# Kernel optimization log

Measured on AMD Instinct MI355X. Metric: run time of the kernel, lower is better.

Reference implementation:

```python
import jax, jax.numpy as jnp
import numpy as np

HIDDEN = 1024
SCALE = float(np.sqrt(HIDDEN))  # canonical sqrt(d) scale factor


def setup_inputs() -> dict:
    key = jax.random.key(0)
    ks = jax.random.split(key, 10)
    B, S, D = 4, 2048, HIDDEN
    bound = 1.0 / np.sqrt(D)  # torch Linear default init range
    inp = {
        "q": jax.random.normal(ks[0], (B, S, D), dtype=jnp.float32),
        "k": jax.random.normal(ks[1], (B, S, D), dtype=jnp.float32),
        "v": jax.random.normal(ks[2], (B, S, D), dtype=jnp.float32),
        "mask": jnp.zeros((B, S, S), dtype=bool),  # unused by original forward
        "Wq": jax.random.uniform(ks[3], (D, D), jnp.float32, -bound, bound),
        "bq": jax.random.uniform(ks[4], (D,), jnp.float32, -bound, bound),
        "Wk": jax.random.uniform(ks[5], (D, D), jnp.float32, -bound, bound),
        "bk": jax.random.uniform(ks[6], (D,), jnp.float32, -bound, bound),
        "Wv": jax.random.uniform(ks[7], (D, D), jnp.float32, -bound, bound),
        "bv": jax.random.uniform(ks[8], (D,), jnp.float32, -bound, bound),
    }
    return inp


def reference(q, k, v, mask, Wq, bq, Wk, bk, Wv, bv):
    # torch Linear: y = x @ W.T + b
    qp = jnp.einsum("bsd,ed->bse", q, Wq) + bq  # [B,S,D]
    kp = jnp.einsum("bsd,ed->bse", k, Wk) + bk
    vp = jnp.einsum("bsd,ed->bse", v, Wv) + bv
    scores = jnp.einsum("bqd,bkd->bqk", qp, kp) / SCALE  # [B,S,S]
    attn = jax.nn.softmax(scores, axis=-1)
    # dropout with p=0 (dropout_p undefined in source) -> identity
    out = jnp.einsum("bqk,bkd->bqd", attn, vp)  # [B,S,D]
    return out
```

## Files before the change

### kernel.cpp

```cpp
#include <hip/hip_runtime.h>

#define S_ 2048
#define D_ 1024
#define MTOT 8192

typedef __attribute__((ext_vector_type(8))) short bf16x8;
typedef __attribute__((ext_vector_type(8))) unsigned short ush8;
typedef __attribute__((ext_vector_type(4))) unsigned short ush4;
typedef __attribute__((ext_vector_type(4))) float f32x4;

__device__ __forceinline__ unsigned short f2bf(float x) {
    unsigned u = __builtin_bit_cast(unsigned, x);
    u += 0x7fffu + ((u >> 16) & 1u);
    return (unsigned short)(u >> 16);
}

__device__ __forceinline__ void async16(const unsigned short* g, unsigned short* l) {
    __builtin_amdgcn_global_load_lds(
        (const __attribute__((address_space(1))) unsigned int*)(g),
        (__attribute__((address_space(3))) unsigned int*)(l),
        16, 0, 0);
}

#define FENCE() asm volatile("" ::: "memory")
#define SBAR()  __builtin_amdgcn_s_barrier()
#define SCHED0() __builtin_amdgcn_sched_barrier(0)

template<int N> __device__ __forceinline__ void waitv();
template<> __device__ __forceinline__ void waitv<0>() { asm volatile("s_waitcnt vmcnt(0)" ::: "memory"); }
template<> __device__ __forceinline__ void waitv<6>() { asm volatile("s_waitcnt vmcnt(6)" ::: "memory"); }
template<> __device__ __forceinline__ void waitv<8>() { asm volatile("s_waitcnt vmcnt(8)" ::: "memory"); }

__device__ __forceinline__ int xcd_remap(int id, int nwg) {
    return (id & 7) * (nwg >> 3) + (id >> 3);
}

__global__ __launch_bounds__(256)
void tobf16_kernel(const float* __restrict__ s0, const float* __restrict__ s1,
                   const float* __restrict__ s2, const float* __restrict__ s3,
                   const float* __restrict__ s4, const float* __restrict__ s5,
                   const float* __restrict__ bq, const float* __restrict__ bk,
                   const float* __restrict__ bv,
                   unsigned short* __restrict__ d0, unsigned short* __restrict__ d1,
                   unsigned short* __restrict__ d2, unsigned short* __restrict__ d3,
                   unsigned short* __restrict__ d4, unsigned short* __restrict__ d5,
                   float* __restrict__ bias_out)
{
    if (blockIdx.y == 6) {
        if (blockIdx.x != 0) return;
        const int t = threadIdx.x;
        for (int i = t; i < 768; i += 256) {
            const int fidx = i * 4;
            const float* src = (fidx < 1024) ? bq : (fidx < 2048) ? bk : bv;
            reinterpret_cast<float4*>(bias_out)[i] =
                reinterpret_cast<const float4*>(src)[(fidx & 1023) >> 2];
        }
        return;
    }
    const float* src; unsigned short* dst; size_t n;
    switch (blockIdx.y) {
        case 0: src = s0; dst = d0; n = (size_t)MTOT * D_; break;
        case 1: src = s1; dst = d1; n = (size_t)MTOT * D_; break;
        case 2: src = s2; dst = d2; n = (size_t)MTOT * D_; break;
        case 3: src = s3; dst = d3; n = (size_t)D_ * D_;   break;
        case 4: src = s4; dst = d4; n = (size_t)D_ * D_;   break;
        default: src = s5; dst = d5; n = (size_t)D_ * D_;  break;
    }
    size_t base = ((size_t)blockIdx.x * 256 + threadIdx.x) * 8;
    if (base >= n) return;
    float4 a = *reinterpret_cast<const float4*>(src + base);
    float4 b = *reinterpret_cast<const float4*>(src + base + 4);
    ush8 h;
    h[0] = f2bf(a.x); h[1] = f2bf(a.y); h[2] = f2bf(a.z); h[3] = f2bf(a.w);
    h[4] = f2bf(b.x); h[5] = f2bf(b.y); h[6] = f2bf(b.z); h[7] = f2bf(b.w);
    *reinterpret_cast<ush8*>(dst + base) = h;
}

template<int EPI, int BM>
__device__ __forceinline__ void gemm_body(
    unsigned short* As, unsigned short* Bs,
    const unsigned short* __restrict__ Ag, int lda,
    const unsigned short* __restrict__ Bg, int ldb,
    const float* __restrict__ bias,
    float* __restrict__ Cf, unsigned short* __restrict__ Cbf,
    int K, float alpha, int ldc, int m0, int n0, size_t coff)
{
    constexpr int WM    = BM / 2;
    constexpr int MI    = WM / 16;
    constexpr int RQ    = MI / 4;
    constexpr int ASLAB = BM / 64;
    constexpr int SC    = ASLAB + 4;
    constexpr int ABUF  = BM * 64;
    constexpr int BBUF  = 256 * 64;

    const int t = threadIdx.x;
    const int w = t >> 6, lane = t & 63;
    const int wr = w >> 2, wc = w & 3;
    const int lr = lane & 15, lk4 = lane >> 4;

    const int crow = t >> 3;
    const int cj = ((lane & 7) ^ ((lane >> 4) & 3) ^ (((lane >> 3) & 1) << 2)) * 8;

    auto stA = [&](int buf, int s, int kt) {
        async16(Ag + (size_t)(m0 + s * 64 + crow) * lda + kt * 64 + cj,
                As + buf * ABUF + s * 4096 + w * 512);
    };
    auto stB = [&](int buf, int s, int kt) {
        async16(Bg + (size_t)(n0 + s * 64 + crow) * ldb + kt * 64 + cj,
                Bs + buf * BBUF + s * 4096 + w * 512);
    };
    auto rdA = [&](int buf, int rr, int kk) -> bf16x8 {
        const int phys = ((kk * 4 + lk4) ^ ((rr >> 1) & 3) ^ ((rr & 1) << 2)) * 8;
        return *reinterpret_cast<const bf16x8*>(As + buf * ABUF + rr * 64 + phys);
    };
    auto rdB = [&](int buf, int rr, int kk) -> bf16x8 {
        const int phys = ((kk * 4 + lk4) ^ ((rr >> 1) & 3) ^ ((rr & 1) << 2)) * 8;
        return *reinterpret_cast<const bf16x8*>(Bs + buf * BBUF + rr * 64 + phys);
    };

    f32x4 acc[MI][4];
    const f32x4 z4 = {0.f, 0.f, 0.f, 0.f};
#pragma unroll
    for (int i = 0; i < MI; i++)
#pragma unroll
        for (int j = 0; j < 4; j++) acc[i][j] = z4;

    const int NT = K >> 6;

#pragma unroll
    for (int s = 0; s < ASLAB; ++s) stA(0, s, 0);
#pragma unroll
    for (int s = 0; s < 4; ++s)     stB(0, s, 0);
#pragma unroll
    for (int s = 0; s < ASLAB; ++s) stA(1, s, 1);
#pragma unroll
    for (int s = 0; s < 4; ++s)     stB(1, s, 1);
    waitv<SC>(); SCHED0(); SBAR(); FENCE();

    for (int kt = 0; kt < NT; ++kt) {
        const int cur = kt & 1;
        const bool pf = (kt + 2 < NT);

        bf16x8 bfr[4][2];
        bf16x8 af[RQ][2];

#pragma unroll
        for (int ni = 0; ni < 4; ++ni)
#pragma unroll
            for (int kk = 0; kk < 2; ++kk)
                bfr[ni][kk] = rdB(cur, wc * 64 + ni * 16 + lr, kk);
#pragma unroll
        for (int rr = 0; rr < RQ; ++rr)
#pragma unroll
            for (int kk = 0; kk < 2; ++kk)
                af[rr][kk] = rdA(cur, wr * WM + rr * 16 + lr, kk);
        FENCE(); SBAR();
        __builtin_amdgcn_s_setprio(1);
#pragma unroll
        for (int rr = 0; rr < RQ; ++rr)
#pragma unroll
            for (int ni = 0; ni < 4; ++ni)
#pragma unroll
                for (int kk = 0; kk < 2; ++kk)
                    acc[rr][ni] = __builtin_amdgcn_mfma_f32_16x16x32_bf16(af[rr][kk], bfr[ni][kk], acc[rr][ni], 0, 0, 0);
        __builtin_amdgcn_s_setprio(0);
        FENCE(); SBAR();

#pragma unroll
        for (int q = 1; q < 4; ++q) {
#pragma unroll
            for (int rr = 0; rr < RQ; ++rr)
#pragma unroll
                for (int kk = 0; kk < 2; ++kk)
                    af[rr][kk] = rdA(cur, wr * WM + (q * RQ + rr) * 16 + lr, kk);
            if (pf) {
                if (q == 1)      { stB(cur, 0, kt + 2); stB(cur, 1, kt + 2); }
                else if (q == 2) { stB(cur, 2, kt + 2); stB(cur, 3, kt + 2); }
                else if (BM == 256) { stA(cur, 0, kt + 2); stA(cur, 2, kt + 2); }
            }
            FENCE(); SBAR();
            __builtin_amdgcn_s_setprio(1);
#pragma unroll
            for (int rr = 0; rr < RQ; ++rr)
#pragma unroll
                for (int ni = 0; ni < 4; ++ni)
#pragma unroll
                    for (int kk = 0; kk < 2; ++kk)
                        acc[q * RQ + rr][ni] = __builtin_amdgcn_mfma_f32_16x16x32_bf16(af[rr][kk], bfr[ni][kk], acc[q * RQ + rr][ni], 0, 0, 0);
            __builtin_amdgcn_s_setprio(0);
            FENCE(); SBAR();
        }

        if (pf) {
            if (BM == 256) { stA(cur, 1, kt + 2); stA(cur, 3, kt + 2); }
            else           { stA(cur, 0, kt + 2); stA(cur, 1, kt + 2); }
            waitv<SC>(); SCHED0(); SBAR(); FENCE();
        } else if (kt + 1 < NT) {
            waitv<0>(); SCHED0(); SBAR(); FENCE();
        }
    }

#pragma unroll
    for (int mi = 0; mi < MI; ++mi) {
        const int mbase = m0 + wr * WM + mi * 16 + lk4 * 4;
#pragma unroll
        for (int ni = 0; ni < 4; ++ni) {
            const int nn = n0 + wc * 64 + ni * 16 + lr;
            if constexpr (EPI == 0) {
#pragma unroll
                for (int r = 0; r < 4; ++r)
                    Cf[coff + (size_t)(mbase + r) * ldc + nn] = alpha * acc[mi][ni][r];
            } else if constexpr (EPI == 1) {
                const float bb = bias[nn];
#pragma unroll
                for (int r = 0; r < 4; ++r)
                    Cbf[(size_t)(mbase + r) * ldc + nn] = f2bf(acc[mi][ni][r] + bb);
            } else {
                const float bb = bias[nn];
                const int nn2 = nn - 2048;
                const int batch = mbase >> 11, ss = mbase & 2047;
                ush4 hv;
#pragma unroll
                for (int r = 0; r < 4; ++r) hv[r] = f2bf(acc[mi][ni][r] + bb);
                *reinterpret_cast<ush4*>(Cbf + ((size_t)(batch << 10) + nn2) * S_ + ss) = hv;
            }
        }
    }
}

__global__ __launch_bounds__(512, 2)
void proj3(const unsigned short* __restrict__ qbf, const unsigned short* __restrict__ kbf,
           const unsigned short* __restrict__ vbf, const unsigned short* __restrict__ wstk,
           const float* __restrict__ bias, unsigned short* __restrict__ QP2,
           unsigned short* __restrict__ vT)
{
    __shared__ unsigned short As[2 * 256 * 64];
    __shared__ unsigned short Bs[2 * 256 * 64];
    int id = xcd_remap(blockIdx.x, 384);
    const int bx = id % 32;
    const int by = id / 32;
    const unsigned short* A = (by < 4) ? qbf : (by < 8) ? kbf : vbf;
    if (by < 8)
        gemm_body<1, 256>(As, Bs, A, D_, wstk, D_, bias, nullptr, QP2,
                          D_, 1.f, 2048, bx * 256, by * 256, 0);
    else
        gemm_body<2, 256>(As, Bs, A, D_, wstk, D_, bias, nullptr, vT,
                          D_, 1.f, 0, bx * 256, by * 256, 0);
}

__global__ __launch_bounds__(512, 2)
void qk256(const unsigned short* __restrict__ QP2, float* __restrict__ sc)
{
    __shared__ unsigned short As[2 * 256 * 64];
    __shared__ unsigned short Bs[2 * 256 * 64];
    int id = xcd_remap(blockIdx.x + 8 * (blockIdx.y + 8 * blockIdx.z), 256);
    const int bx = id % 8; id /= 8;
    const int by = id % 8;
    const int bz = id / 8;
    const unsigned short* base = QP2 + (size_t)bz * S_ * 2048;
    gemm_body<0, 256>(As, Bs, base, 2048, base + 1024, 2048,
                      nullptr, sc, nullptr, D_, 0.03125f, S_,
                      bx * 256, by * 256, (size_t)bz * S_ * S_);
}

__global__ __launch_bounds__(512, 2)
void pv128(const unsigned short* __restrict__ P, const unsigned short* __restrict__ vT,
           float* __restrict__ out)
{
    __shared__ unsigned short As[2 * 128 * 64];
    __shared__ unsigned short Bs[2 * 256 * 64];
    int id = xcd_remap(blockIdx.x + 16 * (blockIdx.y + 4 * blockIdx.z), 256);
    const int bx = id % 16; id /= 16;
    const int by = id % 4;
    const int bz = id / 4;
    gemm_body<0, 128>(As, Bs, P + (size_t)bz * S_ * S_, S_,
                      vT + (size_t)bz * D_ * S_, S_,
                      nullptr, out, nullptr, S_, 1.f, D_,
                      bx * 128, by * 256, (size_t)bz * S_ * D_);
}

__global__ __launch_bounds__(256)
void softmax_kernel(const float* __restrict__ s, unsigned short* __restrict__ P)
{
    const size_t row = blockIdx.x;
    const int t = threadIdx.x;
    const float* sp = s + row * 2048 + (size_t)t * 8;
    float4 a = *reinterpret_cast<const float4*>(sp);
    float4 b = *reinterpret_cast<const float4*>(sp + 4);
    float x[8] = {a.x, a.y, a.z, a.w, b.x, b.y, b.z, b.w};

    float m = x[0];
    for (int j = 1; j < 8; j++) m = fmaxf(m, x[j]);
    for (int off = 1; off < 64; off <<= 1) m = fmaxf(m, __shfl_xor(m, off));
    __shared__ float redm[4], reds[4];
    const int w = t >> 6;
    if ((t & 63) == 0) redm[w] = m;
    __syncthreads();
    m = fmaxf(fmaxf(redm[0], redm[1]), fmaxf(redm[2], redm[3]));

    float e[8]; float sum = 0.f;
    for (int j = 0; j < 8; j++) { e[j] = __expf(x[j] - m); sum += e[j]; }
    for (int off = 1; off < 64; off <<= 1) sum += __shfl_xor(sum, off);
    if ((t & 63) == 0) reds[w] = sum;
    __syncthreads();
    sum = reds[0] + reds[1] + reds[2] + reds[3];
    const float inv = 1.0f / sum;

    ush8 h;
    for (int j = 0; j < 8; j++) h[j] = f2bf(e[j] * inv);
    *reinterpret_cast<ush8*>(P + row * 2048 + (size_t)t * 8) = h;
}

extern "C" void kernel_launch(void* const* d_in, const int* in_sizes, int n_in,
                              void* d_out, int out_size, void* d_ws, size_t ws_size,
                              hipStream_t stream)
{
    const float* q  = (const float*)d_in[0];
    const float* k  = (const float*)d_in[1];
    const float* v  = (const float*)d_in[2];
    const float* Wq = (const float*)d_in[4];
    const float* bq = (const float*)d_in[5];
    const float* Wk = (const float*)d_in[6];
    const float* bk = (const float*)d_in[7];
    const float* Wv = (const float*)d_in[8];
    const float* bv = (const float*)d_in[9];
    float* out = (float*)d_out;

    const size_t MB = (size_t)1 << 20;
    if (ws_size < 200 * MB) return;
    char* ws = (char*)d_ws;
    unsigned short* qbf  = (unsigned short*)(ws + 0 * MB);
    unsigned short* kbf  = (unsigned short*)(ws + 16 * MB);
    unsigned short* vbf  = (unsigned short*)(ws + 32 * MB);
    unsigned short* wstk = (unsigned short*)(ws + 48 * MB);
    float*          bst  = (float*)         (ws + 54 * MB);
    unsigned short* QP2  = (unsigned short*)(ws + 56 * MB);
    unsigned short* vT   = (unsigned short*)(ws + 88 * MB);
    float*          sc   = (float*)         (ws + 104 * MB);
    unsigned short* P    = (unsigned short*)(ws + 168 * MB);

    tobf16_kernel<<<dim3(4096, 7), dim3(256), 0, stream>>>(
        q, k, v, Wq, Wk, Wv, bq, bk, bv,
        qbf, kbf, vbf, wstk, wstk + (size_t)D_ * D_, wstk + 2 * (size_t)D_ * D_, bst);

    proj3<<<dim3(384), dim3(512), 0, stream>>>(qbf, kbf, vbf, wstk, bst, QP2, vT);

    qk256<<<dim3(8, 8, 4), dim3(512), 0, stream>>>(QP2, sc);

    softmax_kernel<<<dim3(MTOT), dim3(256), 0, stream>>>(sc, P);

    pv128<<<dim3(16, 4, 4), dim3(512), 0, stream>>>(P, vT, out);
}
```

Measured before the change: 217.7 us.

## Fuse fp32-to-bf16 activation conversion into projection GEMM A-tile loads

The projection GEMM now reads the fp32 q/k/v activations directly through registers, converts them with packed bf16 conversion instructions and writes them to LDS. This replaces the separate full-tensor bf16 conversion pass and its 48MB intermediate write and read. Weights are still converted by a smaller kernel. The tradeoff is that A tiles are loaded synchronously through registers instead of async global-to-LDS, with twice the global bytes per tile, more register pressure and a changed pipeline schedule.

```diff
diff --git a/kernel.cpp b/kernel.cpp
--- a/kernel.cpp
+++ b/kernel.cpp
@@ -13,6 +13,12 @@
     unsigned u = __builtin_bit_cast(unsigned, x);
     u += 0x7fffu + ((u >> 16) & 1u);
     return (unsigned short)(u >> 16);
+}
+
+__device__ __forceinline__ unsigned cvtpk(float a, float b) {
+    unsigned d;
+    asm("v_cvt_pk_bf16_f32 %0, %1, %2" : "=v"(d) : "v"(a), "v"(b));
+    return d;
 }
 
 __device__ __forceinline__ void async16(const unsigned short* g, unsigned short* l) {
@@ -25,9 +31,11 @@
 #define FENCE() asm volatile("" ::: "memory")
 #define SBAR()  __builtin_amdgcn_s_barrier()
 #define SCHED0() __builtin_amdgcn_sched_barrier(0)
+#define LGKM0() asm volatile("s_waitcnt lgkmcnt(0)" ::: "memory")
 
 template<int N> __device__ __forceinline__ void waitv();
 template<> __device__ __forceinline__ void waitv<0>() { asm volatile("s_waitcnt vmcnt(0)" ::: "memory"); }
+template<> __device__ __forceinline__ void waitv<4>() { asm volatile("s_waitcnt vmcnt(4)" ::: "memory"); }
 template<> __device__ __forceinline__ void waitv<6>() { asm volatile("s_waitcnt vmcnt(6)" ::: "memory"); }
 template<> __device__ __forceinline__ void waitv<8>() { asm volatile("s_waitcnt vmcnt(8)" ::: "memory"); }
 
@@ -36,38 +44,26 @@
 }
 
 __global__ __launch_bounds__(256)
-void tobf16_kernel(const float* __restrict__ s0, const float* __restrict__ s1,
-                   const float* __restrict__ s2, const float* __restrict__ s3,
-                   const float* __restrict__ s4, const float* __restrict__ s5,
-                   const float* __restrict__ bq, const float* __restrict__ bk,
-                   const float* __restrict__ bv,
-                   unsigned short* __restrict__ d0, unsigned short* __restrict__ d1,
-                   unsigned short* __restrict__ d2, unsigned short* __restrict__ d3,
-                   unsigned short* __restrict__ d4, unsigned short* __restrict__ d5,
-                   float* __restrict__ bias_out)
-{
-    if (blockIdx.y == 6) {
+void wconv_kernel(const float* __restrict__ Wq, const float* __restrict__ Wk,
+                  const float* __restrict__ Wv,
+                  const float* __restrict__ bq, const float* __restrict__ bk,
+                  const float* __restrict__ bv,
+                  unsigned short* __restrict__ wstk, float* __restrict__ bst)
+{
+    if (blockIdx.y == 3) {
         if (blockIdx.x != 0) return;
         const int t = threadIdx.x;
         for (int i = t; i < 768; i += 256) {
             const int fidx = i * 4;
             const float* src = (fidx < 1024) ? bq : (fidx < 2048) ? bk : bv;
-            reinterpret_cast<float4*>(bias_out)[i] =
+            reinterpret_cast<float4*>(bst)[i] =
                 reinterpret_cast<const float4*>(src)[(fidx & 1023) >> 2];
         }
         return;
     }
-    const float* src; unsigned short* dst; size_t n;
-    switch (blockIdx.y) {
-        case 0: src = s0; dst = d0; n = (size_t)MTOT * D_; break;
-        case 1: src = s1; dst = d1; n = (size_t)MTOT * D_; break;
-        case 2: src = s2; dst = d2; n = (size_t)MTOT * D_; break;
-        case 3: src = s3; dst = d3; n = (size_t)D_ * D_;   break;
-        case 4: src = s4; dst = d4; n = (size_t)D_ * D_;   break;
-        default: src = s5; dst = d5; n = (size_t)D_ * D_;  break;
-    }
+    const float* src = (blockIdx.y == 0) ? Wq : (blockIdx.y == 1) ? Wk : Wv;
+    unsigned short* dst = wstk + (size_t)blockIdx.y * D_ * D_;
     size_t base = ((size_t)blockIdx.x * 256 + threadIdx.x) * 8;
-    if (base >= n) return;
     float4 a = *reinterpret_cast<const float4*>(src + base);
     float4 b = *reinterpret_cast<const float4*>(src + base + 4);
     ush8 h;
@@ -76,10 +72,10 @@
     *reinterpret_cast<ush8*>(dst + base) = h;
 }
 
-template<int EPI, int BM>
+template<int EPI, int BM, bool AF32>
 __device__ __forceinline__ void gemm_body(
     unsigned short* As, unsigned short* Bs,
-    const unsigned short* __restrict__ Ag, int lda,
+    const void* Agv, int lda,
     const unsigned short* __restrict__ Bg, int ldb,
     const float* __restrict__ bias,
     float* __restrict__ Cf, unsigned short* __restrict__ Cbf,
@@ -93,6 +89,9 @@
     constexpr int ABUF  = BM * 64;
     constexpr int BBUF  = 256 * 64;
 
+    const unsigned short* Ag = (const unsigned short*)Agv;
+    const float*          Af = (const float*)Agv;
+
     const int t = threadIdx.x;
     const int w = t >> 6, lane = t & 63;
     const int wr = w >> 2, wc = w & 3;
@@ -118,6 +117,27 @@
         return *reinterpret_cast<const bf16x8*>(Bs + buf * BBUF + rr * 64 + phys);
     };
 
+    float4 ar[4][2];
+    auto issueA = [&](int kt) {
+#pragma unroll
+        for (int s = 0; s < 4; ++s) {
+            const float* p = Af + (size_t)(m0 + s * 64 + crow) * lda + kt * 64 + cj;
+            ar[s][0] = *reinterpret_cast<const float4*>(p);
+            ar[s][1] = *reinterpret_cast<const float4*>(p + 4);
+        }
+    };
+    auto writeA = [&](int buf) {
+#pragma unroll
+        for (int s = 0; s < 4; ++s) {
+            uint4 v;
+            v.x = cvtpk(ar[s][0].x, ar[s][0].y);
+            v.y = cvtpk(ar[s][0].z, ar[s][0].w);
+            v.z = cvtpk(ar[s][1].x, ar[s][1].y);
+            v.w = cvtpk(ar[s][1].z, ar[s][1].w);
+            *reinterpret_cast<uint4*>(As + buf * ABUF + s * 4096 + w * 512 + lane * 8) = v;
+        }
+    };
+
     f32x4 acc[MI][4];
     const f32x4 z4 = {0.f, 0.f, 0.f, 0.f};
 #pragma unroll
@@ -127,15 +147,46 @@
 
     const int NT = K >> 6;
 
-#pragma unroll
-    for (int s = 0; s < ASLAB; ++s) stA(0, s, 0);
-#pragma unroll
-    for (int s = 0; s < 4; ++s)     stB(0, s, 0);
-#pragma unroll
-    for (int s = 0; s < ASLAB; ++s) stA(1, s, 1);
-#pragma unroll
-    for (int s = 0; s < 4; ++s)     stB(1, s, 1);
-    waitv<SC>(); SCHED0(); SBAR(); FENCE();
+    if constexpr (AF32) {
+        float4 arP[4][2];
+#pragma unroll
+        for (int s = 0; s < 4; ++s) {
+            const float* p = Af + (size_t)(m0 + s * 64 + crow) * lda + 0 * 64 + cj;
+            arP[s][0] = *reinterpret_cast<const float4*>(p);
+            arP[s][1] = *reinterpret_cast<const float4*>(p + 4);
+        }
+        SCHED0();
+        issueA(1);
+        SCHED0();
+#pragma unroll
+        for (int s = 0; s < 4; ++s) stB(0, s, 0);
+#pragma unroll
+        for (int s = 0; s < 4; ++s) stB(1, s, 1);
+        waitv<8>();
+#pragma unroll
+        for (int s = 0; s < 4; ++s) {
+            uint4 v;
+            v.x = cvtpk(arP[s][0].x, arP[s][0].y);
+            v.y = cvtpk(arP[s][0].z, arP[s][0].w);
+            v.z = cvtpk(arP[s][1].x, arP[s][1].y);
+            v.w = cvtpk(arP[s][1].z, arP[s][1].w);
+            *reinterpret_cast<uint4*>(As + 0 * ABUF + s * 4096 + w * 512 + lane * 8) = v;
+        }
+        writeA(1);
+        LGKM0();
+        waitv<4>();
+        SCHED0(); SBAR(); FENCE();
+    } else {
+#pragma unroll
+        for (int s = 0; s < ASLAB; ++s) stA(0, s, 0);
+#pragma unroll
+        for (int s = 0; s < 4; ++s)     stB(0, s, 0);
+#pragma unroll
+        for (int s = 0; s < ASLAB; ++s) stA(1, s, 1);
+#pragma unroll
+        for (int s = 0; s < 4; ++s)     stB(1, s, 1);
+        waitv<SC>(); SCHED0(); SBAR(); FENCE();
+    }
 
     for (int kt = 0; kt < NT; ++kt) {
         const int cur = kt & 1;
@@ -154,6 +205,9 @@
 #pragma unroll
             for (int kk = 0; kk < 2; ++kk)
                 af[rr][kk] = rdA(cur, wr * WM + rr * 16 + lr, kk);
+        if constexpr (AF32) {
+            if (pf) { issueA(kt + 2); SCHED0(); }
+        }
         FENCE(); SBAR();
         __builtin_amdgcn_s_setprio(1);
 #pragma unroll
@@ -176,7 +230,7 @@
             if (pf) {
                 if (q == 1)      { stB(cur, 0, kt + 2); stB(cur, 1, kt + 2); }
                 else if (q == 2) { stB(cur, 2, kt + 2); stB(cur, 3, kt + 2); }
-                else if (BM == 256) { stA(cur, 0, kt + 2); stA(cur, 2, kt + 2); }
+                else if (!AF32 && BM == 256) { stA(cur, 0, kt + 2); stA(cur, 2, kt + 2); }
             }
             FENCE(); SBAR();
             __builtin_amdgcn_s_setprio(1);
@@ -191,12 +245,23 @@
             FENCE(); SBAR();
         }
 
-        if (pf) {
-            if (BM == 256) { stA(cur, 1, kt + 2); stA(cur, 3, kt + 2); }
-            else           { stA(cur, 0, kt + 2); stA(cur, 1, kt + 2); }
-            waitv<SC>(); SCHED0(); SBAR(); FENCE();
-        } else if (kt + 1 < NT) {
-            waitv<0>(); SCHED0(); SBAR(); FENCE();
+        if constexpr (AF32) {
+            if (pf) {
+                waitv<4>();
+                writeA(cur);
+                LGKM0();
+                SCHED0(); SBAR(); FENCE();
+            } else if (kt + 1 < NT) {
+                waitv<0>(); SCHED0(); SBAR(); FENCE();
+            }
+        } else {
+            if (pf) {
+                if (BM == 256) { stA(cur, 1, kt + 2); stA(cur, 3, kt + 2); }
+                else           { stA(cur, 0, kt + 2); stA(cur, 1, kt + 2); }
+                waitv<SC>(); SCHED0(); SBAR(); FENCE();
+            } else if (kt + 1 < NT) {
+                waitv<0>(); SCHED0(); SBAR(); FENCE();
+            }
         }
     }
 
@@ -229,8 +294,8 @@
 }
 
 __global__ __launch_bounds__(512, 2)
-void proj3(const unsigned short* __restrict__ qbf, const unsigned short* __restrict__ kbf,
-           const unsigned short* __restrict__ vbf, const unsigned short* __restrict__ wstk,
+void proj3(const float* __restrict__ q, const float* __restrict__ k,
+           const float* __restrict__ v, const unsigned short* __restrict__ wstk,
            const float* __restrict__ bias, unsigned short* __restrict__ QP2,
            unsigned short* __restrict__ vT)
 {
@@ -239,13 +304,13 @@
     int id = xcd_remap(blockIdx.x, 384);
     const int bx = id % 32;
     const int by = id / 32;
-    const unsigned short* A = (by < 4) ? qbf : (by < 8) ? kbf : vbf;
+    const float* A = (by < 4) ? q : (by < 8) ? k : v;
     if (by < 8)
-        gemm_body<1, 256>(As, Bs, A, D_, wstk, D_, bias, nullptr, QP2,
-                          D_, 1.f, 2048, bx * 256, by * 256, 0);
+        gemm_body<1, 256, true>(As, Bs, A, D_, wstk, D_, bias, nullptr, QP2,
+                                D_, 1.f, 2048, bx * 256, by * 256, 0);
     else
-        gemm_body<2, 256>(As, Bs, A, D_, wstk, D_, bias, nullptr, vT,
-                          D_, 1.f, 0, bx * 256, by * 256, 0);
+        gemm_body<2, 256, true>(As, Bs, A, D_, wstk, D_, bias, nullptr, vT,
+                                D_, 1.f, 0, bx * 256, by * 256, 0);
 }
 
 __global__ __launch_bounds__(512, 2)
@@ -258,9 +323,9 @@
     const int by = id % 8;
     const int bz = id / 8;
     const unsigned short* base = QP2 + (size_t)bz * S_ * 2048;
-    gemm_body<0, 256>(As, Bs, base, 2048, base + 1024, 2048,
-                      nullptr, sc, nullptr, D_, 0.03125f, S_,
-                      bx * 256, by * 256, (size_t)bz * S_ * S_);
+    gemm_body<0, 256, false>(As, Bs, base, 2048, base + 1024, 2048,
+                             nullptr, sc, nullptr, D_, 0.03125f, S_,
+                             bx * 256, by * 256, (size_t)bz * S_ * S_);
 }
 
 __global__ __launch_bounds__(512, 2)
@@ -273,10 +338,10 @@
     const int bx = id % 16; id /= 16;
     const int by = id % 4;
     const int bz = id / 4;
-    gemm_body<0, 128>(As, Bs, P + (size_t)bz * S_ * S_, S_,
-                      vT + (size_t)bz * D_ * S_, S_,
-                      nullptr, out, nullptr, S_, 1.f, D_,
-                      bx * 128, by * 256, (size_t)bz * S_ * D_);
+    gemm_body<0, 128, false>(As, Bs, P + (size_t)bz * S_ * S_, S_,
+                             vT + (size_t)bz * D_ * S_, S_,
+                             nullptr, out, nullptr, S_, 1.f, D_,
+                             bx * 128, by * 256, (size_t)bz * S_ * D_);
 }
 
 __global__ __launch_bounds__(256)
@@ -327,23 +392,18 @@
     float* out = (float*)d_out;
 
     const size_t MB = (size_t)1 << 20;
-    if (ws_size < 200 * MB) return;
+    if (ws_size < 152 * MB) return;
     char* ws = (char*)d_ws;
-    unsigned short* qbf  = (unsigned short*)(ws + 0 * MB);
-    unsigned short* kbf  = (unsigned short*)(ws + 16 * MB);
-    unsigned short* vbf  = (unsigned short*)(ws + 32 * MB);
-    unsigned short* wstk = (unsigned short*)(ws + 48 * MB);
-    float*          bst  = (float*)         (ws + 54 * MB);
-    unsigned short* QP2  = (unsigned short*)(ws + 56 * MB);
-    unsigned short* vT   = (unsigned short*)(ws + 88 * MB);
-    float*          sc   = (float*)         (ws + 104 * MB);
-    unsigned short* P    = (unsigned short*)(ws + 168 * MB);
-
-    tobf16_kernel<<<dim3(4096, 7), dim3(256), 0, stream>>>(
-        q, k, v, Wq, Wk, Wv, bq, bk, bv,
-        qbf, kbf, vbf, wstk, wstk + (size_t)D_ * D_, wstk + 2 * (size_t)D_ * D_, bst);
-
-    proj3<<<dim3(384), dim3(512), 0, stream>>>(qbf, kbf, vbf, wstk, bst, QP2, vT);
+    unsigned short* wstk = (unsigned short*)(ws + 0 * MB);
+    float*          bst  = (float*)         (ws + 6 * MB);
+    unsigned short* QP2  = (unsigned short*)(ws + 8 * MB);
+    unsigned short* vT   = (unsigned short*)(ws + 40 * MB);
+    float*          sc   = (float*)         (ws + 56 * MB);
+    unsigned short* P    = (unsigned short*)(ws + 120 * MB);
+
+    wconv_kernel<<<dim3(512, 4), dim3(256), 0, stream>>>(Wq, Wk, Wv, bq, bk, bv, wstk, bst);
+
+    proj3<<<dim3(384), dim3(512), 0, stream>>>(q, k, v, wstk, bst, QP2, vT);
 
     qk256<<<dim3(8, 8, 4), dim3(512), 0, stream>>>(QP2, sc);
 
```

Result: slower. 228.3 us (+4.9%).
